# Optimization experiments

Hardware: AMD Instinct MI355X
Metric: run time of the kernel (lower is better)

The kernel has to match this reference:

```python
import jax, jax.numpy as jnp
import numpy as np

NUM_CLASSES = 1000
DIM = 256
N = 400000
MOMENTUM = 0.9


def setup_inputs() -> dict:
    key = jax.random.key(0)
    k1, k2, k3 = jax.random.split(key, 3)
    grads = jax.random.normal(k1, (N, DIM), dtype=jnp.float32)
    labels = jax.random.randint(k2, (N,), 0, NUM_CLASSES)
    # centroids buffer in its steady (initialized=True) state
    centroids = jax.random.normal(k3, (NUM_CLASSES, DIM), dtype=jnp.float32) * 0.1
    return {"grads": grads, "labels": labels, "centroids": centroids}


def reference(grads, labels, centroids):
    # --- update_centroids: per-class masked mean + EMA, as one segment-reduce ---
    sums = jax.ops.segment_sum(grads, labels, num_segments=NUM_CLASSES)            # [C, D]
    counts = jax.ops.segment_sum(jnp.ones((grads.shape[0],), grads.dtype), labels,
                                 num_segments=NUM_CLASSES)                          # [C]
    class_means = sums / jnp.maximum(counts, 1.0)[:, None]                          # [C, D]
    present = (counts > 0)[:, None]
    new_centroids = jnp.where(present,
                              MOMENTUM * centroids + (1.0 - MOMENTUM) * class_means,
                              centroids)                                            # classes with no samples keep old centroid

    # --- purify: rank-1 projection removing the first principal direction ---
    centered = new_centroids - new_centroids.mean(axis=0, keepdims=True)            # [C, D]
    _, _, Vh = jnp.linalg.svd(centered, full_matrices=False)
    v_y = Vh[0]                                                                     # [D]
    proj = (grads @ v_y)[:, None] * v_y[None, :]                                    # [N, D]
    return grads - proj
```

## Files before the change

kernel.cpp:

```cpp
#include <hip/hip_runtime.h>

#define N_ROWS 400000
#define DIM 256
#define NCLS 1000
#define NSQ 10

#define NB_S 256
#define NT_S 512
#define NBE  128
#define NTE  1024
#define NB_P 2048
#define NT_P 256
#define TOTW_P (NB_P * (NT_P / 64))

#define OFF_BAR     0
#define OFF_BAR2    64
#define OFF_COUNTS  1024
#define OFF_COLSUM  5120
#define OFF_MAXBUF  6144
#define ZERO_BYTES  6208
#define OFF_BASE    6208
#define OFF_CURSOR  10304
#define OFF_V       14400
#define OFF_IDX     15424
#define OFF_NC      1615424
#define OFF_MA      2639424
#define OFF_MB      2901568

template <int NBLK>
__device__ __forceinline__ void grid_bar(unsigned* bar, int& phase) {
  __syncthreads();
  if (threadIdx.x == 0) {
    ++phase;
    __threadfence();
    __hip_atomic_fetch_add(bar, 1u, __ATOMIC_RELAXED, __HIP_MEMORY_SCOPE_AGENT);
    const unsigned target = (unsigned)NBLK * (unsigned)phase;
    while (__hip_atomic_load(bar, __ATOMIC_RELAXED, __HIP_MEMORY_SCOPE_AGENT) < target)
      __builtin_amdgcn_s_sleep(8);
    __threadfence();
  }
  __syncthreads();
}

__global__ __launch_bounds__(NT_S) void k_sort(const int* __restrict__ labels,
                                               char* __restrict__ ws) {
  unsigned* bar    = (unsigned*)(ws + OFF_BAR);
  unsigned* counts = (unsigned*)(ws + OFF_COUNTS);
  unsigned* base   = (unsigned*)(ws + OFF_BASE);
  unsigned* cursor = (unsigned*)(ws + OFF_CURSOR);
  unsigned* idx    = (unsigned*)(ws + OFF_IDX);

  __shared__ unsigned su[1024];
  const int t = threadIdx.x, b = blockIdx.x;
  int phase = 0;

  for (int i = t; i < NCLS; i += NT_S) su[i] = 0u;
  __syncthreads();
  for (int i = b*NT_S + t; i < N_ROWS; i += NB_S*NT_S)
    atomicAdd(&su[labels[i]], 1u);
  __syncthreads();
  for (int i = t; i < NCLS; i += NT_S) { unsigned v = su[i]; if (v) atomicAdd(&counts[i], v); }
  grid_bar<NB_S>(bar, phase);

  if (b == 0) {
    su[t] = counts[t]; su[t+512] = counts[t+512];
    int offset = 1;
    for (int d = 512; d > 0; d >>= 1) {
      __syncthreads();
      if (t < d) { int ai = offset*(2*t+1)-1, bi = offset*(2*t+2)-1; su[bi] += su[ai]; }
      offset <<= 1;
    }
    __syncthreads();
    if (t == 0) su[1023] = 0u;
    for (int d = 1; d < 1024; d <<= 1) {
      offset >>= 1;
      __syncthreads();
      if (t < d) { int ai = offset*(2*t+1)-1, bi = offset*(2*t+2)-1;
                   unsigned tm = su[ai]; su[ai] = su[bi]; su[bi] += tm; }
    }
    __syncthreads();
    base[t] = su[t]; cursor[t] = su[t];
    base[t+512] = su[t+512]; cursor[t+512] = su[t+512];
  }
  grid_bar<NB_S>(bar, phase);

  for (int i = b*NT_S + t; i < N_ROWS; i += NB_S*NT_S) {
    unsigned p = atomicAdd(&cursor[labels[i]], 1u);
    idx[p] = (unsigned)i;
  }
}

__global__ __launch_bounds__(512) void k_reduce(const float* __restrict__ grads,
                                                const unsigned* __restrict__ idx,
                                                const unsigned* __restrict__ base,
                                                const unsigned* __restrict__ counts,
                                                const float* __restrict__ centroids,
                                                float* __restrict__ NC,
                                                float* __restrict__ colsum) {
  const int cls = blockIdx.x;
  const unsigned s0 = base[cls], n = counts[cls];
  const int wave = threadIdx.x >> 6, lane = threadIdx.x & 63;
  const float4* g4 = (const float4*)grads;
  float4 acc = make_float4(0.f, 0.f, 0.f, 0.f);
  unsigned u = (unsigned)wave;
  for (; u + 8 < n; u += 16) {
    unsigned r0 = idx[s0+u], r1 = idx[s0+u+8];
    float4 a = g4[(size_t)r0*64 + lane];
    float4 c = g4[(size_t)r1*64 + lane];
    acc.x += a.x + c.x; acc.y += a.y + c.y;
    acc.z += a.z + c.z; acc.w += a.w + c.w;
  }
  for (; u < n; u += 8) {
    unsigned r0 = idx[s0+u];
    float4 a = g4[(size_t)r0*64 + lane];
    acc.x += a.x; acc.y += a.y; acc.z += a.z; acc.w += a.w;
  }
  __shared__ float4 tmp[8][64];
  tmp[wave][lane] = acc;
  __syncthreads();
  const int d = threadIdx.x;
  if (d < DIM) {
    const float* tf = (const float*)tmp;
    float s = 0.f;
    #pragma unroll
    for (int w2 = 0; w2 < 8; ++w2) s += tf[w2*256 + d];
    float mean = s / fmaxf((float)n, 1.0f);
    float ce = centroids[cls*DIM + d];
    float ncv = (n > 0u) ? (0.9f*ce + 0.1f*mean) : ce;
    NC[cls*DIM + d] = ncv;
    atomicAdd(&colsum[d], ncv);
  }
}

__global__ __launch_bounds__(NTE) void k_eigen(char* __restrict__ ws) {
  unsigned* bar2   = (unsigned*)(ws + OFF_BAR2);
  float*    colsum = (float*)(ws + OFF_COLSUM);
  unsigned* maxbuf = (unsigned*)(ws + OFF_MAXBUF);
  float*    vfin   = (float*)(ws + OFF_V);
  float*    NC     = (float*)(ws + OFF_NC);
  float*    MA     = (float*)(ws + OFF_MA);
  float*    MB     = (float*)(ws + OFF_MB);

  __shared__ float scol[2][NCLS];
  __shared__ float sf[2][NTE];
  __shared__ float sx[DIM], sy[DIM];
  __shared__ int   sidx[256];
  __shared__ unsigned smax;

  const int t = threadIdx.x, b = blockIdx.x;
  const int i = t & 255, h = t >> 8;
  int phase = 0;

  {
    const int j0 = b, j1 = b + NBE;
    if (t < NCLS) { scol[0][t] = NC[t*DIM + j0]; scol[1][t] = NC[t*DIM + j1]; }
    if (t == 0) smax = 0u;
    __syncthreads();
    float a0 = 0.f, a1 = 0.f;
    const int k0 = h * 250;
    #pragma unroll 5
    for (int k = k0; k < k0 + 250; ++k) {
      float nv = NC[k*DIM + i];
      a0 += nv * scol[0][k];
      a1 += nv * scol[1][k];
    }
    sf[0][t] = a0; sf[1][t] = a1;
    __syncthreads();
    if (h == 0) {
      float v0 = sf[0][i]+sf[0][i+256]+sf[0][i+512]+sf[0][i+768] - colsum[i]*colsum[j0]*(1.0f/NCLS);
      float v1 = sf[1][i]+sf[1][i+256]+sf[1][i+512]+sf[1][i+768] - colsum[i]*colsum[j1]*(1.0f/NCLS);
      MA[j0*DIM + i] = v0;
      MA[j1*DIM + i] = v1;
      float am = fmaxf(fabsf(v0), fabsf(v1));
      #pragma unroll
      for (int m = 1; m < 64; m <<= 1) am = fmaxf(am, __shfl_xor(am, m, 64));
      if ((t & 63) == 0) atomicMax(&smax, __float_as_uint(am));
    }
    __syncthreads();
    if (t == 0) atomicMax(maxbuf, smax);
  }
  grid_bar<NBE>(bar2, phase);

  for (int st = 0; st < NSQ; ++st) {
    const float* A = (st & 1) ? MB : MA;
    float*       C = (st & 1) ? MA : MB;
    const float inv = 1.0f / __uint_as_float(maxbuf[st]);
    const int j0 = b, j1 = b + NBE;
    if (t < DIM) { scol[0][t] = A[j0*DIM + t]; scol[1][t] = A[j1*DIM + t]; }
    if (t == 0) smax = 0u;
    __syncthreads();
    float a0 = 0.f, a1 = 0.f;
    const int k0 = h * 64;
    #pragma unroll 8
    for (int k = k0; k < k0 + 64; ++k) {
      float av = A[k*DIM + i];
      a0 += av * scol[0][k];
      a1 += av * scol[1][k];
    }
    sf[0][t] = a0; sf[1][t] = a1;
    __syncthreads();
    if (h == 0) {
      float v0 = (sf[0][i]+sf[0][i+256]+sf[0][i+512]+sf[0][i+768]) * inv * inv;
      float v1 = (sf[1][i]+sf[1][i+256]+sf[1][i+512]+sf[1][i+768]) * inv * inv;
      C[j0*DIM + i] = v0;
      C[j1*DIM + i] = v1;
      float am = fmaxf(fabsf(v0), fabsf(v1));
      #pragma unroll
      for (int m = 1; m < 64; m <<= 1) am = fmaxf(am, __shfl_xor(am, m, 64));
      if ((t & 63) == 0) atomicMax(&smax, __float_as_uint(am));
    }
    __syncthreads();
    if (t == 0) atomicMax(&maxbuf[st+1], smax);
    grid_bar<NBE>(bar2, phase);
  }

  if (b == 0) {
    const int k0 = h * 64;
    float ns = 0.f;
    for (int k = k0; k < k0 + 64; ++k) { float x = MA[k*DIM + i]; ns += x*x; }
    sf[0][t] = ns;
    __syncthreads();
    if (h == 0) {
      scol[0][i] = sf[0][i]+sf[0][i+256]+sf[0][i+512]+sf[0][i+768];
      sidx[i] = i;
    }
    __syncthreads();
    for (int s = 128; s > 0; s >>= 1) {
      if (t < s && scol[0][t+s] > scol[0][t]) { scol[0][t] = scol[0][t+s]; sidx[t] = sidx[t+s]; }
      __syncthreads();
    }
    const int jm = sidx[0];
    const float nrm = sqrtf(fmaxf(scol[0][0], 1e-30f));
    __syncthreads();
    if (t < DIM) sx[t] = MA[(size_t)jm*DIM + t] / nrm;
    __syncthreads();
    for (int it = 0; it < 3; ++it) {
      float a2 = 0.f;
      #pragma unroll 8
      for (int k = k0; k < k0 + 64; ++k) a2 += MA[k*DIM + i] * sx[k];
      sf[0][t] = a2;
      __syncthreads();
      if (h == 0) {
        float yv = sf[0][i]+sf[0][i+256]+sf[0][i+512]+sf[0][i+768];
        sy[i] = yv;
        float q = yv*yv;
        #pragma unroll
        for (int m = 1; m < 64; m <<= 1) q += __shfl_xor(q, m, 64);
        if ((i & 63) == 0) scol[0][i >> 6] = q;
      }
      __syncthreads();
      const float innrm = rsqrtf(fmaxf(scol[0][0]+scol[0][1]+scol[0][2]+scol[0][3], 1e-30f));
      if (t < DIM) sx[t] = sy[t] * innrm;
      __syncthreads();
    }
    if (t < DIM) vfin[t] = sx[t];
  }
}

__global__ __launch_bounds__(NT_P) void k_project(const float4* __restrict__ g4,
                                                  const float* __restrict__ v,
                                                  float4* __restrict__ out) {
  const int lane = threadIdx.x & 63;
  const float4 v4 = ((const float4*)v)[lane];
  const int w = blockIdx.x * (NT_P/64) + (threadIdx.x >> 6);
  int r = w;
  for (; r + TOTW_P < N_ROWS; r += 2*TOTW_P) {
    float4 a = g4[(size_t)r*64 + lane];
    float4 c = g4[(size_t)(r+TOTW_P)*64 + lane];
    float da = a.x*v4.x + a.y*v4.y + a.z*v4.z + a.w*v4.w;
    float db = c.x*v4.x + c.y*v4.y + c.z*v4.z + c.w*v4.w;
    #pragma unroll
    for (int m = 1; m < 64; m <<= 1) { da += __shfl_xor(da, m, 64); db += __shfl_xor(db, m, 64); }
    out[(size_t)r*64 + lane] = make_float4(a.x-da*v4.x, a.y-da*v4.y, a.z-da*v4.z, a.w-da*v4.w);
    out[(size_t)(r+TOTW_P)*64 + lane] = make_float4(c.x-db*v4.x, c.y-db*v4.y, c.z-db*v4.z, c.w-db*v4.w);
  }
  for (; r < N_ROWS; r += TOTW_P) {
    float4 a = g4[(size_t)r*64 + lane];
    float da = a.x*v4.x + a.y*v4.y + a.z*v4.z + a.w*v4.w;
    #pragma unroll
    for (int m = 1; m < 64; m <<= 1) da += __shfl_xor(da, m, 64);
    out[(size_t)r*64 + lane] = make_float4(a.x-da*v4.x, a.y-da*v4.y, a.z-da*v4.z, a.w-da*v4.w);
  }
}

extern "C" void kernel_launch(void* const* d_in, const int* in_sizes, int n_in,
                              void* d_out, int out_size, void* d_ws, size_t ws_size,
                              hipStream_t stream) {
  const float* grads     = (const float*)d_in[0];
  const int*   labels    = (const int*)d_in[1];
  const float* centroids = (const float*)d_in[2];
  float* out = (float*)d_out;
  char* ws = (char*)d_ws;

  unsigned* idx    = (unsigned*)(ws + OFF_IDX);
  unsigned* counts = (unsigned*)(ws + OFF_COUNTS);
  unsigned* base   = (unsigned*)(ws + OFF_BASE);
  float*    colsum = (float*)(ws + OFF_COLSUM);
  float*    vfin   = (float*)(ws + OFF_V);
  float*    NC     = (float*)(ws + OFF_NC);

  hipMemsetAsync(ws, 0, ZERO_BYTES, stream);

  k_sort<<<NB_S, NT_S, 0, stream>>>(labels, ws);
  k_reduce<<<NCLS, 512, 0, stream>>>(grads, idx, base, counts, centroids, NC, colsum);
  k_eigen<<<NBE, NTE, 0, stream>>>(ws);
  k_project<<<NB_P, NT_P, 0, stream>>>((const float4*)grads, vfin, (float4*)out);
}
```

Baseline: 528.6 us.

## Halve eigen grid, cut squarings, add transposed centroids, nontemporal projection IO

```diff
diff --git a/kernel.cpp b/kernel.cpp
--- a/kernel.cpp
+++ b/kernel.cpp
@@ -3,15 +3,17 @@
 #define N_ROWS 400000
 #define DIM 256
 #define NCLS 1000
-#define NSQ 10
+#define NSQ 8
 
 #define NB_S 256
 #define NT_S 512
-#define NBE  128
+#define NBE  64
 #define NTE  1024
 #define NB_P 2048
 #define NT_P 256
 #define TOTW_P (NB_P * (NT_P / 64))
+
+typedef float f4 __attribute__((ext_vector_type(4)));
 
 #define OFF_BAR     0
 #define OFF_BAR2    64
@@ -24,8 +26,9 @@
 #define OFF_V       14400
 #define OFF_IDX     15424
 #define OFF_NC      1615424
-#define OFF_MA      2639424
-#define OFF_MB      2901568
+#define OFF_NCT     2639424
+#define OFF_MA      3663424
+#define OFF_MB      3925568
 
 template <int NBLK>
 __device__ __forceinline__ void grid_bar(unsigned* bar, int& phase) {
@@ -96,6 +99,7 @@
                                                 const unsigned* __restrict__ counts,
                                                 const float* __restrict__ centroids,
                                                 float* __restrict__ NC,
+                                                float* __restrict__ NCT,
                                                 float* __restrict__ colsum) {
   const int cls = blockIdx.x;
   const unsigned s0 = base[cls], n = counts[cls];
@@ -103,12 +107,17 @@
   const float4* g4 = (const float4*)grads;
   float4 acc = make_float4(0.f, 0.f, 0.f, 0.f);
   unsigned u = (unsigned)wave;
-  for (; u + 8 < n; u += 16) {
-    unsigned r0 = idx[s0+u], r1 = idx[s0+u+8];
+  for (; u + 24 < n; u += 32) {
+    unsigned r0 = idx[s0+u],    r1 = idx[s0+u+8];
+    unsigned r2 = idx[s0+u+16], r3 = idx[s0+u+24];
     float4 a = g4[(size_t)r0*64 + lane];
     float4 c = g4[(size_t)r1*64 + lane];
-    acc.x += a.x + c.x; acc.y += a.y + c.y;
-    acc.z += a.z + c.z; acc.w += a.w + c.w;
+    float4 d = g4[(size_t)r2*64 + lane];
+    float4 e = g4[(size_t)r3*64 + lane];
+    acc.x += (a.x + c.x) + (d.x + e.x);
+    acc.y += (a.y + c.y) + (d.y + e.y);
+    acc.z += (a.z + c.z) + (d.z + e.z);
+    acc.w += (a.w + c.w) + (d.w + e.w);
   }
   for (; u < n; u += 8) {
     unsigned r0 = idx[s0+u];
@@ -127,7 +136,8 @@
     float mean = s / fmaxf((float)n, 1.0f);
     float ce = centroids[cls*DIM + d];
     float ncv = (n > 0u) ? (0.9f*ce + 0.1f*mean) : ce;
-    NC[cls*DIM + d] = ncv;
+    NC[cls*DIM + d]  = ncv;
+    NCT[d*NCLS + cls] = ncv;
     atomicAdd(&colsum[d], ncv);
   }
 }
@@ -138,11 +148,12 @@
   unsigned* maxbuf = (unsigned*)(ws + OFF_MAXBUF);
   float*    vfin   = (float*)(ws + OFF_V);
   float*    NC     = (float*)(ws + OFF_NC);
+  float*    NCT    = (float*)(ws + OFF_NCT);
   float*    MA     = (float*)(ws + OFF_MA);
   float*    MB     = (float*)(ws + OFF_MB);
 
-  __shared__ float scol[2][NCLS];
-  __shared__ float sf[2][NTE];
+  __shared__ float scol[4][NCLS];
+  __shared__ float sf[4][NTE];
   __shared__ float sx[DIM], sy[DIM];
   __shared__ int   sidx[256];
   __shared__ unsigned smax;
@@ -152,26 +163,31 @@
   int phase = 0;
 
   {
-    const int j0 = b, j1 = b + NBE;
-    if (t < NCLS) { scol[0][t] = NC[t*DIM + j0]; scol[1][t] = NC[t*DIM + j1]; }
+    #pragma unroll
+    for (int q = 0; q < 4; ++q)
+      if (t < NCLS) scol[q][t] = NCT[(size_t)(b + 64*q)*NCLS + t];
     if (t == 0) smax = 0u;
     __syncthreads();
-    float a0 = 0.f, a1 = 0.f;
+    float a0 = 0.f, a1 = 0.f, a2 = 0.f, a3 = 0.f;
     const int k0 = h * 250;
     #pragma unroll 5
     for (int k = k0; k < k0 + 250; ++k) {
       float nv = NC[k*DIM + i];
-      a0 += nv * scol[0][k];
-      a1 += nv * scol[1][k];
-    }
-    sf[0][t] = a0; sf[1][t] = a1;
+      a0 += nv * scol[0][k]; a1 += nv * scol[1][k];
+      a2 += nv * scol[2][k]; a3 += nv * scol[3][k];
+    }
+    sf[0][t] = a0; sf[1][t] = a1; sf[2][t] = a2; sf[3][t] = a3;
     __syncthreads();
     if (h == 0) {
-      float v0 = sf[0][i]+sf[0][i+256]+sf[0][i+512]+sf[0][i+768] - colsum[i]*colsum[j0]*(1.0f/NCLS);
-      float v1 = sf[1][i]+sf[1][i+256]+sf[1][i+512]+sf[1][i+768] - colsum[i]*colsum[j1]*(1.0f/NCLS);
-      MA[j0*DIM + i] = v0;
-      MA[j1*DIM + i] = v1;
-      float am = fmaxf(fabsf(v0), fabsf(v1));
+      float am = 0.f;
+      #pragma unroll
+      for (int q = 0; q < 4; ++q) {
+        const int j = b + 64*q;
+        float v = sf[q][i]+sf[q][i+256]+sf[q][i+512]+sf[q][i+768]
+                - colsum[i]*colsum[j]*(1.0f/NCLS);
+        MA[j*DIM + i] = v;
+        am = fmaxf(am, fabsf(v));
+      }
       #pragma unroll
       for (int m = 1; m < 64; m <<= 1) am = fmaxf(am, __shfl_xor(am, m, 64));
       if ((t & 63) == 0) atomicMax(&smax, __float_as_uint(am));
@@ -185,26 +201,30 @@
     const float* A = (st & 1) ? MB : MA;
     float*       C = (st & 1) ? MA : MB;
     const float inv = 1.0f / __uint_as_float(maxbuf[st]);
-    const int j0 = b, j1 = b + NBE;
-    if (t < DIM) { scol[0][t] = A[j0*DIM + t]; scol[1][t] = A[j1*DIM + t]; }
+    #pragma unroll
+    for (int q = 0; q < 4; ++q)
+      if (t < DIM) scol[q][t] = A[(b + 64*q)*DIM + t];
     if (t == 0) smax = 0u;
     __syncthreads();
-    float a0 = 0.f, a1 = 0.f;
+    float a0 = 0.f, a1 = 0.f, a2 = 0.f, a3 = 0.f;
     const int k0 = h * 64;
     #pragma unroll 8
     for (int k = k0; k < k0 + 64; ++k) {
       float av = A[k*DIM + i];
-      a0 += av * scol[0][k];
-      a1 += av * scol[1][k];
-    }
-    sf[0][t] = a0; sf[1][t] = a1;
+      a0 += av * scol[0][k]; a1 += av * scol[1][k];
+      a2 += av * scol[2][k]; a3 += av * scol[3][k];
+    }
+    sf[0][t] = a0; sf[1][t] = a1; sf[2][t] = a2; sf[3][t] = a3;
     __syncthreads();
     if (h == 0) {
-      float v0 = (sf[0][i]+sf[0][i+256]+sf[0][i+512]+sf[0][i+768]) * inv * inv;
-      float v1 = (sf[1][i]+sf[1][i+256]+sf[1][i+512]+sf[1][i+768]) * inv * inv;
-      C[j0*DIM + i] = v0;
-      C[j1*DIM + i] = v1;
-      float am = fmaxf(fabsf(v0), fabsf(v1));
+      float am = 0.f;
+      #pragma unroll
+      for (int q = 0; q < 4; ++q) {
+        const int j = b + 64*q;
+        float v = (sf[q][i]+sf[q][i+256]+sf[q][i+512]+sf[q][i+768]) * inv * inv;
+        C[j*DIM + i] = v;
+        am = fmaxf(am, fabsf(v));
+      }
       #pragma unroll
       for (int m = 1; m < 64; m <<= 1) am = fmaxf(am, __shfl_xor(am, m, 64));
       if ((t & 63) == 0) atomicMax(&smax, __float_as_uint(am));
@@ -257,29 +277,32 @@
   }
 }
 
-__global__ __launch_bounds__(NT_P) void k_project(const float4* __restrict__ g4,
+__global__ __launch_bounds__(NT_P) void k_project(const f4* __restrict__ g4,
                                                   const float* __restrict__ v,
-                                                  float4* __restrict__ out) {
+                                                  f4* __restrict__ out) {
   const int lane = threadIdx.x & 63;
-  const float4 v4 = ((const float4*)v)[lane];
+  const f4 v4 = ((const f4*)v)[lane];
   const int w = blockIdx.x * (NT_P/64) + (threadIdx.x >> 6);
   int r = w;
   for (; r + TOTW_P < N_ROWS; r += 2*TOTW_P) {
-    float4 a = g4[(size_t)r*64 + lane];
-    float4 c = g4[(size_t)(r+TOTW_P)*64 + lane];
+    f4 a = __builtin_nontemporal_load(&g4[(size_t)r*64 + lane]);
+    f4 c = __builtin_nontemporal_load(&g4[(size_t)(r+TOTW_P)*64 + lane]);
     float da = a.x*v4.x + a.y*v4.y + a.z*v4.z + a.w*v4.w;
     float db = c.x*v4.x + c.y*v4.y + c.z*v4.z + c.w*v4.w;
     #pragma unroll
     for (int m = 1; m < 64; m <<= 1) { da += __shfl_xor(da, m, 64); db += __shfl_xor(db, m, 64); }
-    out[(size_t)r*64 + lane] = make_float4(a.x-da*v4.x, a.y-da*v4.y, a.z-da*v4.z, a.w-da*v4.w);
-    out[(size_t)(r+TOTW_P)*64 + lane] = make_float4(c.x-db*v4.x, c.y-db*v4.y, c.z-db*v4.z, c.w-db*v4.w);
+    f4 o0 = a - da * v4;
+    f4 o1 = c - db * v4;
+    __builtin_nontemporal_store(o0, &out[(size_t)r*64 + lane]);
+    __builtin_nontemporal_store(o1, &out[(size_t)(r+TOTW_P)*64 + lane]);
   }
   for (; r < N_ROWS; r += TOTW_P) {
-    float4 a = g4[(size_t)r*64 + lane];
+    f4 a = __builtin_nontemporal_load(&g4[(size_t)r*64 + lane]);
     float da = a.x*v4.x + a.y*v4.y + a.z*v4.z + a.w*v4.w;
     #pragma unroll
     for (int m = 1; m < 64; m <<= 1) da += __shfl_xor(da, m, 64);
-    out[(size_t)r*64 + lane] = make_float4(a.x-da*v4.x, a.y-da*v4.y, a.z-da*v4.z, a.w-da*v4.w);
+    f4 o = a - da * v4;
+    __builtin_nontemporal_store(o, &out[(size_t)r*64 + lane]);
   }
 }
 
@@ -298,11 +321,12 @@
   float*    colsum = (float*)(ws + OFF_COLSUM);
   float*    vfin   = (float*)(ws + OFF_V);
   float*    NC     = (float*)(ws + OFF_NC);
-
-  hipMemsetAsync(ws, 0, ZERO_BYTES, stream);
+  float*    NCT    = (float*)(ws + OFF_NCT);
+
+  (void)hipMemsetAsync(ws, 0, ZERO_BYTES, stream);
 
   k_sort<<<NB_S, NT_S, 0, stream>>>(labels, ws);
-  k_reduce<<<NCLS, 512, 0, stream>>>(grads, idx, base, counts, centroids, NC, colsum);
+  k_reduce<<<NCLS, 512, 0, stream>>>(grads, idx, base, counts, centroids, NC, NCT, colsum);
   k_eigen<<<NBE, NTE, 0, stream>>>(ws);
-  k_project<<<NB_P, NT_P, 0, stream>>>((const float4*)grads, vfin, (float4*)out);
-}
+  k_project<<<NB_P, NT_P, 0, stream>>>((const f4*)grads, vfin, (f4*)out);
+}
```

Result: faster. 440.1 us (-16.8%).
